# Kernel tuning notes

Measured on AMD Instinct MI355X. Metric: run time of the kernel, lower is better.

Reference implementation:

```python
import jax, jax.numpy as jnp
import numpy as np

EPS = 1e-7


def setup_inputs() -> dict:
    key = jax.random.key(0)
    kx, kw, kv, kp = jax.random.split(key, 4)
    B, H, Wd, d, V, O = 4, 64, 64, 64, 64, 64
    X = jax.random.normal(kx, (B, H, Wd, d), dtype=jnp.float32)
    W = jax.random.normal(kw, (d, V), dtype=jnp.float32)
    # positive variances (kmeans-style init in original); avoid near-zero divisors
    variance = jax.random.uniform(kv, (d, V), dtype=jnp.float32) + 0.5
    weight = jax.random.normal(kp, (d, O), dtype=jnp.float32) * (1.0 / np.sqrt(d))
    return {"X": X, "W": W, "variance": variance, "weight": weight}


def reference(X, W, variance, weight):
    B, H, Wd, d = X.shape
    V = W.shape[1]
    HW = H * Wd
    Xf = X.reshape(B, HW, d)
    # Faithful replication of torch code: extend = tile(X, V) over last axis,
    # then reshape (d*V) -> (d, V) with k = a*V + c, so the X component at
    # grid position (a, c) is X[..., (a*V + c) % d].
    idx = (jnp.arange(d)[:, None] * V + jnp.arange(V)[None, :]) % d  # (d, V)
    Xg = Xf[:, :, idx]                      # (B, HW, d, V)
    q1 = (Xg - W) / variance                # (B, HW, d, V), broadcast (d,V)
    q = jnp.sum(q1 * q1, axis=2)            # (B, HW, V) squared Mahalanobis-ish dist
    q = q - jnp.min(q, axis=-1, keepdims=True)
    Q = jnp.exp(-0.5 * q)
    Q = Q / jnp.sum(Q, axis=-1, keepdims=True)          # soft assignment (B, HW, V)
    # Raw row-major reinterpretation (B, HW, d*V) -> (B, d, HW, V), as in torch
    z = q1.reshape(B, d, HW, V)
    zQ = z * Q[:, None, :, :]                            # (B, d, HW, V)
    z = jnp.sum(zQ, axis=2)                              # (B, d, V)
    Qsum = jnp.sum(Q, axis=1)                            # (B, V)
    z = (z + EPS) / (Qsum[:, None, :] + EPS)
    norm = jnp.sum(z * z, axis=1, keepdims=True)         # (B, 1, V)
    Z = z / norm                                          # (B, d, V)
    Adj = jnp.einsum('bdv,bdu->bvu', Z, Z)               # (B, V, V)
    out = jnp.einsum('bdv,do->bvo', Z, weight)           # (B, V, O)
    out = jnp.einsum('bvu,buo->bvo', Adj, out)           # (B, V, O)
    Zo = jax.nn.relu(out)
    Xn = jnp.einsum('bnv,bvo->bno', Q, Zo)               # (B, HW, O)
    return Xn.reshape(B, H, Wd, -1).transpose(0, 3, 1, 2)  # (B, O, H, W)
```

## Files before the change

### kernel.cpp

```cpp
#include <hip/hip_runtime.h>

#define HW 4096
#define EPSF 1e-7f

#define WS_S1  0
#define WS_S2P 16384
#define WS_QSP 32768
#define WS_Z   49152
#define WS_ZO  65536
#define WS_ABC 81920

__device__ __forceinline__ void xr4(float4& v) {
    v.x += __shfl_xor(v.x, 16); v.y += __shfl_xor(v.y, 16);
    v.z += __shfl_xor(v.z, 16); v.w += __shfl_xor(v.w, 16);
    v.x += __shfl_xor(v.x, 32); v.y += __shfl_xor(v.y, 32);
    v.z += __shfl_xor(v.z, 32); v.w += __shfl_xor(v.w, 32);
}

__device__ __forceinline__ float4 row_softmax(float4 x, float4 A4, float4 B4, float4 C4) {
    float4 q;
    q.x = fmaf(fmaf(A4.x, x.x, -2.0f * B4.x), x.x, C4.x);
    q.y = fmaf(fmaf(A4.y, x.y, -2.0f * B4.y), x.y, C4.y);
    q.z = fmaf(fmaf(A4.z, x.z, -2.0f * B4.z), x.z, C4.z);
    q.w = fmaf(fmaf(A4.w, x.w, -2.0f * B4.w), x.w, C4.w);
    float m = fminf(fminf(q.x, q.y), fminf(q.z, q.w));
    m = fminf(m, __shfl_xor(m, 1)); m = fminf(m, __shfl_xor(m, 2));
    m = fminf(m, __shfl_xor(m, 4)); m = fminf(m, __shfl_xor(m, 8));
    float4 e;
    e.x = __expf(-0.5f * (q.x - m)); e.y = __expf(-0.5f * (q.y - m));
    e.z = __expf(-0.5f * (q.z - m)); e.w = __expf(-0.5f * (q.w - m));
    float s = e.x + e.y + e.z + e.w;
    s += __shfl_xor(s, 1); s += __shfl_xor(s, 2);
    s += __shfl_xor(s, 4); s += __shfl_xor(s, 8);
    float rs = 1.0f / s;
    float4 Q4; Q4.x = e.x * rs; Q4.y = e.y * rs; Q4.z = e.z * rs; Q4.w = e.w * rs;
    return Q4;
}

__global__ __launch_bounds__(512) void kA(const float* __restrict__ X,
                                          const float* __restrict__ Wm,
                                          const float* __restrict__ var,
                                          float* __restrict__ ws) {
    int b = blockIdx.x >> 6, l = blockIdx.x & 63;
    int t = threadIdx.x;
    int wv = t >> 6, j = t & 63;
    int lane16 = t & 15, r0 = t >> 4;
    __shared__ float4 red4[3][8][16];
    __shared__ float4 abc4[3][16];

    float4 iv0, iv1, wiv0, wiv1;
    float4 aA = {0,0,0,0}, aB = {0,0,0,0}, aC = {0,0,0,0};
    {
        float4 v4 = *(const float4*)&var[r0 * 64 + lane16 * 4];
        float4 w4 = *(const float4*)&Wm[r0 * 64 + lane16 * 4];
        iv0.x = 1.0f / v4.x; iv0.y = 1.0f / v4.y; iv0.z = 1.0f / v4.z; iv0.w = 1.0f / v4.w;
        wiv0.x = w4.x * iv0.x; wiv0.y = w4.y * iv0.y; wiv0.z = w4.z * iv0.z; wiv0.w = w4.w * iv0.w;
        aA.x = fmaf(iv0.x, iv0.x, aA.x); aA.y = fmaf(iv0.y, iv0.y, aA.y);
        aA.z = fmaf(iv0.z, iv0.z, aA.z); aA.w = fmaf(iv0.w, iv0.w, aA.w);
        aB.x = fmaf(wiv0.x, iv0.x, aB.x); aB.y = fmaf(wiv0.y, iv0.y, aB.y);
        aB.z = fmaf(wiv0.z, iv0.z, aB.z); aB.w = fmaf(wiv0.w, iv0.w, aB.w);
        aC.x = fmaf(wiv0.x, wiv0.x, aC.x); aC.y = fmaf(wiv0.y, wiv0.y, aC.y);
        aC.z = fmaf(wiv0.z, wiv0.z, aC.z); aC.w = fmaf(wiv0.w, wiv0.w, aC.w);
    }
    {
        int i = r0 + 32;
        float4 v4 = *(const float4*)&var[i * 64 + lane16 * 4];
        float4 w4 = *(const float4*)&Wm[i * 64 + lane16 * 4];
        iv1.x = 1.0f / v4.x; iv1.y = 1.0f / v4.y; iv1.z = 1.0f / v4.z; iv1.w = 1.0f / v4.w;
        wiv1.x = w4.x * iv1.x; wiv1.y = w4.y * iv1.y; wiv1.z = w4.z * iv1.z; wiv1.w = w4.w * iv1.w;
        aA.x = fmaf(iv1.x, iv1.x, aA.x); aA.y = fmaf(iv1.y, iv1.y, aA.y);
        aA.z = fmaf(iv1.z, iv1.z, aA.z); aA.w = fmaf(iv1.w, iv1.w, aA.w);
        aB.x = fmaf(wiv1.x, iv1.x, aB.x); aB.y = fmaf(wiv1.y, iv1.y, aB.y);
        aB.z = fmaf(wiv1.z, iv1.z, aB.z); aB.w = fmaf(wiv1.w, iv1.w, aB.w);
        aC.x = fmaf(wiv1.x, wiv1.x, aC.x); aC.y = fmaf(wiv1.y, wiv1.y, aC.y);
        aC.z = fmaf(wiv1.z, wiv1.z, aC.z); aC.w = fmaf(wiv1.w, wiv1.w, aC.w);
    }
    xr4(aA); xr4(aB); xr4(aC);
    if ((t & 63) < 16) { red4[0][wv][lane16] = aA; red4[1][wv][lane16] = aB; red4[2][wv][lane16] = aC; }
    __syncthreads();
    if (t < 16) {
        float4 A = {0,0,0,0}, Bq = {0,0,0,0}, C = {0,0,0,0};
#pragma unroll
        for (int w = 0; w < 8; w++) {
            float4 a = red4[0][w][t], bb = red4[1][w][t], c = red4[2][w][t];
            A.x += a.x; A.y += a.y; A.z += a.z; A.w += a.w;
            Bq.x += bb.x; Bq.y += bb.y; Bq.z += bb.z; Bq.w += bb.w;
            C.x += c.x; C.y += c.y; C.z += c.z; C.w += c.w;
        }
        abc4[0][t] = A; abc4[1][t] = Bq; abc4[2][t] = C;
        if (blockIdx.x == 0) {
            *(float4*)&ws[WS_ABC + t * 4]       = A;
            *(float4*)&ws[WS_ABC + 64 + t * 4]  = Bq;
            *(float4*)&ws[WS_ABC + 128 + t * 4] = C;
        }
    }
    __syncthreads();
    float4 A4 = abc4[0][lane16], B4 = abc4[1][lane16], C4 = abc4[2][lane16];

    float4 s1 = {0,0,0,0}, s2 = {0,0,0,0}, qsm = {0,0,0,0};
    {
        int n = l * 64 + r0;
        float4 x = *(const float4*)&X[((size_t)(b * HW) + n) * 64 + lane16 * 4];
        float4 Q4 = row_softmax(x, A4, B4, C4);
        s1.x = fmaf(iv0.x, Q4.x, s1.x); s1.y = fmaf(iv0.y, Q4.y, s1.y);
        s1.z = fmaf(iv0.z, Q4.z, s1.z); s1.w = fmaf(iv0.w, Q4.w, s1.w);
        s2.x = fmaf(wiv0.x, Q4.x, s2.x); s2.y = fmaf(wiv0.y, Q4.y, s2.y);
        s2.z = fmaf(wiv0.z, Q4.z, s2.z); s2.w = fmaf(wiv0.w, Q4.w, s2.w);
        qsm.x += Q4.x; qsm.y += Q4.y; qsm.z += Q4.z; qsm.w += Q4.w;
    }
    {
        int n = l * 64 + r0 + 32;
        float4 x = *(const float4*)&X[((size_t)(b * HW) + n) * 64 + lane16 * 4];
        float4 Q4 = row_softmax(x, A4, B4, C4);
        s1.x = fmaf(iv1.x, Q4.x, s1.x); s1.y = fmaf(iv1.y, Q4.y, s1.y);
        s1.z = fmaf(iv1.z, Q4.z, s1.z); s1.w = fmaf(iv1.w, Q4.w, s1.w);
        s2.x = fmaf(wiv1.x, Q4.x, s2.x); s2.y = fmaf(wiv1.y, Q4.y, s2.y);
        s2.z = fmaf(wiv1.z, Q4.z, s2.z); s2.w = fmaf(wiv1.w, Q4.w, s2.w);
        qsm.x += Q4.x; qsm.y += Q4.y; qsm.z += Q4.z; qsm.w += Q4.w;
    }
    xr4(s1); xr4(s2); xr4(qsm);
    __syncthreads();
    if ((t & 63) < 16) { red4[0][wv][lane16] = s1; red4[1][wv][lane16] = s2; red4[2][wv][lane16] = qsm; }
    __syncthreads();
    if (t < 64) {
        int jg = j >> 2, cc = j & 3;
        float t0 = 0.f, t1 = 0.f, t2 = 0.f;
#pragma unroll
        for (int w = 0; w < 8; w++) {
            t0 += ((const float*)&red4[0][w][jg])[cc];
            t1 += ((const float*)&red4[1][w][jg])[cc];
            t2 += ((const float*)&red4[2][w][jg])[cc];
        }
        int idx = (b * 64 + l) * 64 + j;
        ws[WS_S1  + idx] = t0;
        ws[WS_S2P + idx] = t1;
        ws[WS_QSP + idx] = t2;
    }
}

__global__ __launch_bounds__(512) void kB(const float* __restrict__ X,
                                          float* __restrict__ ws) {
    int b = blockIdx.x >> 6, h = blockIdx.x & 63;
    int t = threadIdx.x;
    int wv = t >> 6, j = t & 63;
    int lane16 = t & 15, lg = t >> 4;
    __shared__ float4 red4[3][8][16];
    float4 acc = {0,0,0,0}, ps2 = {0,0,0,0}, pqs = {0,0,0,0};
#pragma unroll
    for (int half = 0; half < 2; half++) {
        int l = lg + half * 32;
        float4 x  = *(const float4*)&X[((size_t)(b * HW) + h * 64 + l) * 64 + lane16 * 4];
        int idx = (b * 64 + l) * 64 + lane16 * 4;
        float4 s1 = *(const float4*)&ws[WS_S1 + idx];
        float4 a2 = *(const float4*)&ws[WS_S2P + idx];
        float4 a3 = *(const float4*)&ws[WS_QSP + idx];
        acc.x = fmaf(x.x, s1.x, acc.x); acc.y = fmaf(x.y, s1.y, acc.y);
        acc.z = fmaf(x.z, s1.z, acc.z); acc.w = fmaf(x.w, s1.w, acc.w);
        ps2.x += a2.x; ps2.y += a2.y; ps2.z += a2.z; ps2.w += a2.w;
        pqs.x += a3.x; pqs.y += a3.y; pqs.z += a3.z; pqs.w += a3.w;
    }
    xr4(acc); xr4(ps2); xr4(pqs);
    if ((t & 63) < 16) {
        red4[0][wv][lane16] = acc; red4[1][wv][lane16] = ps2; red4[2][wv][lane16] = pqs;
    }
    __syncthreads();
    if (t < 64) {
        int jg = j >> 2, cc = j & 3;
        float a = 0.f, s2 = 0.f, q = 0.f;
#pragma unroll
        for (int w = 0; w < 8; w++) {
            a  += ((const float*)&red4[0][w][jg])[cc];
            s2 += ((const float*)&red4[1][w][jg])[cc];
            q  += ((const float*)&red4[2][w][jg])[cc];
        }
        ws[WS_Z + (b * 64 + h) * 64 + j] = (a - s2 + EPSF) / (q + EPSF);
    }
}

__global__ __launch_bounds__(512) void kCD(const float* __restrict__ weight,
                                           float* __restrict__ ws) {
    int b = blockIdx.x >> 6, v = blockIdx.x & 63;
    int w8 = threadIdx.x >> 6, j = threadIdx.x & 63;
    __shared__ float zl[64][65];
    __shared__ float wl[64][65];
    __shared__ float red[8][64];
    __shared__ float sN[64], sin2[64], ghat[64], yv[64];
#pragma unroll
    for (int k = 0; k < 2; k++) {
        int fidx = (k * 512 + threadIdx.x) * 4;
        int r = fidx >> 6, cc = fidx & 63;
        float4 zv = *(const float4*)&ws[WS_Z + b * 4096 + fidx];
        float4 wv = *(const float4*)&weight[fidx];
        zl[r][cc] = zv.x; zl[r][cc+1] = zv.y; zl[r][cc+2] = zv.z; zl[r][cc+3] = zv.w;
        wl[r][cc] = wv.x; wl[r][cc+1] = wv.y; wl[r][cc+2] = wv.z; wl[r][cc+3] = wv.w;
    }
    __syncthreads();
    {
        float na = 0.f;
#pragma unroll
        for (int k = 0; k < 8; k++) { float zz = zl[w8 * 8 + k][j]; na = fmaf(zz, zz, na); }
        red[w8][j] = na;
        __syncthreads();
        if (threadIdx.x < 64) {
            float s = 0.f;
#pragma unroll
            for (int tt = 0; tt < 8; tt++) s += red[tt][j];
            sN[j] = s; sin2[j] = 1.0f / (s * s);
        }
        __syncthreads();
    }
    {
        float g = 0.f;
#pragma unroll
        for (int k = 0; k < 8; k++) { int d = w8 * 8 + k; g = fmaf(zl[d][v], zl[d][j], g); }
        red[w8][j] = g;
        __syncthreads();
        if (threadIdx.x < 64) {
            float s = 0.f;
#pragma unroll
            for (int tt = 0; tt < 8; tt++) s += red[tt][j];
            ghat[j] = s * sin2[j];
        }
        __syncthreads();
    }
    {
        float y = 0.f;
#pragma unroll
        for (int k = 0; k < 8; k++) { int u = w8 * 8 + k; y = fmaf(ghat[u], zl[j][u], y); }
        red[w8][j] = y;
        __syncthreads();
        if (threadIdx.x < 64) {
            float s = 0.f;
#pragma unroll
            for (int tt = 0; tt < 8; tt++) s += red[tt][j];
            yv[j] = s;
        }
        __syncthreads();
    }
    {
        float a = 0.f;
#pragma unroll
        for (int k = 0; k < 8; k++) { int d = w8 * 8 + k; a = fmaf(yv[d], wl[d][j], a); }
        red[w8][j] = a;
        __syncthreads();
        if (threadIdx.x < 64) {
            float s = 0.f;
#pragma unroll
            for (int tt = 0; tt < 8; tt++) s += red[tt][j];
            float r = s / sN[v];
            r = r > 0.f ? r : 0.f;
            ws[WS_ZO + (b * 64 + v) * 64 + j] = r;
        }
    }
}

__global__ __launch_bounds__(512) void kF(const float* __restrict__ X,
                                          const float* __restrict__ ws,
                                          float* __restrict__ out) {
    int b = blockIdx.x >> 6, tb = blockIdx.x & 63;
    int nbase = tb * 64;
    int t = threadIdx.x;
    int w8 = t >> 6, j = t & 63;
    int lane16 = t & 15, r0 = t >> 4;
    int o8 = w8 * 8;
    __shared__ float qs[64][65];
    __shared__ __align__(16) float zo[64][68];

    float4 A4 = *(const float4*)&ws[WS_ABC + lane16 * 4];
    float4 B4 = *(const float4*)&ws[WS_ABC + 64 + lane16 * 4];
    float4 C4 = *(const float4*)&ws[WS_ABC + 128 + lane16 * 4];

#pragma unroll
    for (int k = 0; k < 2; k++) {
        int fidx = (k * 512 + t) * 4;
        int r = fidx >> 6, cc = fidx & 63;
        float4 zv = *(const float4*)&ws[WS_ZO + b * 4096 + fidx];
        zo[r][cc] = zv.x; zo[r][cc+1] = zv.y; zo[r][cc+2] = zv.z; zo[r][cc+3] = zv.w;
    }
#pragma unroll
    for (int half = 0; half < 2; half++) {
        int rr = r0 + half * 32;
        int n = nbase + rr;
        float4 x = *(const float4*)&X[((size_t)(b * HW) + n) * 64 + lane16 * 4];
        float4 Q4 = row_softmax(x, A4, B4, C4);
        qs[rr][lane16 * 4]     = Q4.x;
        qs[rr][lane16 * 4 + 1] = Q4.y;
        qs[rr][lane16 * 4 + 2] = Q4.z;
        qs[rr][lane16 * 4 + 3] = Q4.w;
    }
    __syncthreads();

    float acc[8];
#pragma unroll
    for (int k = 0; k < 8; k++) acc[k] = 0.f;
#pragma unroll
    for (int v = 0; v < 64; v++) {
        float qv = qs[j][v];
        float4 z0 = *(const float4*)&zo[v][o8];
        float4 z1 = *(const float4*)&zo[v][o8 + 4];
        acc[0] = fmaf(qv, z0.x, acc[0]);
        acc[1] = fmaf(qv, z0.y, acc[1]);
        acc[2] = fmaf(qv, z0.z, acc[2]);
        acc[3] = fmaf(qv, z0.w, acc[3]);
        acc[4] = fmaf(qv, z1.x, acc[4]);
        acc[5] = fmaf(qv, z1.y, acc[5]);
        acc[6] = fmaf(qv, z1.z, acc[6]);
        acc[7] = fmaf(qv, z1.w, acc[7]);
    }
#pragma unroll
    for (int k = 0; k < 8; k++) {
        int o = o8 + k;
        out[(size_t)(b * 64 + o) * HW + nbase + j] = acc[k];
    }
}

extern "C" void kernel_launch(void* const* d_in, const int* in_sizes, int n_in,
                              void* d_out, int out_size, void* d_ws, size_t ws_size,
                              hipStream_t stream) {
    const float* X      = (const float*)d_in[0];
    const float* Wm     = (const float*)d_in[1];
    const float* var    = (const float*)d_in[2];
    const float* weight = (const float*)d_in[3];
    float* ws  = (float*)d_ws;
    float* out = (float*)d_out;

    kA <<<256, 512, 0, stream>>>(X, Wm, var, ws);
    kB <<<256, 512, 0, stream>>>(X, ws);
    kCD<<<256, 512, 0, stream>>>(weight, ws);
    kF <<<256, 512, 0, stream>>>(X, ws, out);
}
```

Before: 21.69 us.

## Fuse kB and kCD into one launch with per-batch atomic counters

Merges the Z-reduction kernel and the adjacency/projection kernel into a single 512-block launch. The first 256 blocks compute Z and bump a per-batch counter, and the other 256 blocks spin on that counter before doing the CD work. Counters are zeroed in kA. This removes one kernel launch boundary, but it relies on producer blocks being scheduled before or alongside the spinning consumer blocks, and polling adds its own latency.

```diff
diff --git a/kernel.cpp b/kernel.cpp
--- a/kernel.cpp
+++ b/kernel.cpp
@@ -9,6 +9,7 @@
 #define WS_Z   49152
 #define WS_ZO  65536
 #define WS_ABC 81920
+#define WS_CTR 82176
 
 __device__ __forceinline__ void xr4(float4& v) {
     v.x += __shfl_xor(v.x, 16); v.y += __shfl_xor(v.y, 16);
@@ -48,6 +49,8 @@
     __shared__ float4 red4[3][8][16];
     __shared__ float4 abc4[3][16];
 
+    if (blockIdx.x == 0 && t < 8) ((int*)(ws + WS_CTR))[t] = 0;
+
     float4 iv0, iv1, wiv0, wiv1;
     float4 aA = {0,0,0,0}, aB = {0,0,0,0}, aC = {0,0,0,0};
     {
@@ -138,116 +141,137 @@
     }
 }
 
-__global__ __launch_bounds__(512) void kB(const float* __restrict__ X,
-                                          float* __restrict__ ws) {
-    int b = blockIdx.x >> 6, h = blockIdx.x & 63;
-    int t = threadIdx.x;
-    int wv = t >> 6, j = t & 63;
-    int lane16 = t & 15, lg = t >> 4;
-    __shared__ float4 red4[3][8][16];
-    float4 acc = {0,0,0,0}, ps2 = {0,0,0,0}, pqs = {0,0,0,0};
-#pragma unroll
-    for (int half = 0; half < 2; half++) {
-        int l = lg + half * 32;
-        float4 x  = *(const float4*)&X[((size_t)(b * HW) + h * 64 + l) * 64 + lane16 * 4];
-        int idx = (b * 64 + l) * 64 + lane16 * 4;
-        float4 s1 = *(const float4*)&ws[WS_S1 + idx];
-        float4 a2 = *(const float4*)&ws[WS_S2P + idx];
-        float4 a3 = *(const float4*)&ws[WS_QSP + idx];
-        acc.x = fmaf(x.x, s1.x, acc.x); acc.y = fmaf(x.y, s1.y, acc.y);
-        acc.z = fmaf(x.z, s1.z, acc.z); acc.w = fmaf(x.w, s1.w, acc.w);
-        ps2.x += a2.x; ps2.y += a2.y; ps2.z += a2.z; ps2.w += a2.w;
-        pqs.x += a3.x; pqs.y += a3.y; pqs.z += a3.z; pqs.w += a3.w;
-    }
-    xr4(acc); xr4(ps2); xr4(pqs);
-    if ((t & 63) < 16) {
-        red4[0][wv][lane16] = acc; red4[1][wv][lane16] = ps2; red4[2][wv][lane16] = pqs;
-    }
-    __syncthreads();
-    if (t < 64) {
-        int jg = j >> 2, cc = j & 3;
-        float a = 0.f, s2 = 0.f, q = 0.f;
-#pragma unroll
-        for (int w = 0; w < 8; w++) {
-            a  += ((const float*)&red4[0][w][jg])[cc];
-            s2 += ((const float*)&red4[1][w][jg])[cc];
-            q  += ((const float*)&red4[2][w][jg])[cc];
-        }
-        ws[WS_Z + (b * 64 + h) * 64 + j] = (a - s2 + EPSF) / (q + EPSF);
-    }
-}
-
-__global__ __launch_bounds__(512) void kCD(const float* __restrict__ weight,
-                                           float* __restrict__ ws) {
-    int b = blockIdx.x >> 6, v = blockIdx.x & 63;
-    int w8 = threadIdx.x >> 6, j = threadIdx.x & 63;
-    __shared__ float zl[64][65];
-    __shared__ float wl[64][65];
-    __shared__ float red[8][64];
-    __shared__ float sN[64], sin2[64], ghat[64], yv[64];
+struct BRole { float4 red4[3][8][16]; };
+struct CDRole {
+    float zl[64][65]; float wl[64][65];
+    float red[8][64];
+    float sN[64]; float sin2[64]; float ghat[64]; float yv[64];
+};
+union SMU { BRole b; CDRole c; };
+
+__global__ __launch_bounds__(512) void kBCD(const float* __restrict__ X,
+                                            const float* __restrict__ weight,
+                                            float* __restrict__ ws) {
+    __shared__ SMU sm;
+    int* ctr = (int*)(ws + WS_CTR);
+    const int t = threadIdx.x;
+
+    if (blockIdx.x < 256) {
+        int b = blockIdx.x >> 6, h = blockIdx.x & 63;
+        int wv = t >> 6, j = t & 63;
+        int lane16 = t & 15, lg = t >> 4;
+        float4 acc = {0,0,0,0}, ps2 = {0,0,0,0}, pqs = {0,0,0,0};
+#pragma unroll
+        for (int half = 0; half < 2; half++) {
+            int l = lg + half * 32;
+            float4 x  = *(const float4*)&X[((size_t)(b * HW) + h * 64 + l) * 64 + lane16 * 4];
+            int idx = (b * 64 + l) * 64 + lane16 * 4;
+            float4 s1 = *(const float4*)&ws[WS_S1 + idx];
+            float4 a2 = *(const float4*)&ws[WS_S2P + idx];
+            float4 a3 = *(const float4*)&ws[WS_QSP + idx];
+            acc.x = fmaf(x.x, s1.x, acc.x); acc.y = fmaf(x.y, s1.y, acc.y);
+            acc.z = fmaf(x.z, s1.z, acc.z); acc.w = fmaf(x.w, s1.w, acc.w);
+            ps2.x += a2.x; ps2.y += a2.y; ps2.z += a2.z; ps2.w += a2.w;
+            pqs.x += a3.x; pqs.y += a3.y; pqs.z += a3.z; pqs.w += a3.w;
+        }
+        xr4(acc); xr4(ps2); xr4(pqs);
+        if ((t & 63) < 16) {
+            sm.b.red4[0][wv][lane16] = acc; sm.b.red4[1][wv][lane16] = ps2; sm.b.red4[2][wv][lane16] = pqs;
+        }
+        __syncthreads();
+        if (t < 64) {
+            int jg = j >> 2, cc = j & 3;
+            float a = 0.f, s2 = 0.f, q = 0.f;
+#pragma unroll
+            for (int w = 0; w < 8; w++) {
+                a  += ((const float*)&sm.b.red4[0][w][jg])[cc];
+                s2 += ((const float*)&sm.b.red4[1][w][jg])[cc];
+                q  += ((const float*)&sm.b.red4[2][w][jg])[cc];
+            }
+            ws[WS_Z + (b * 64 + h) * 64 + j] = (a - s2 + EPSF) / (q + EPSF);
+        }
+        __syncthreads();
+        if (t == 0) {
+            __threadfence();
+            __hip_atomic_fetch_add(ctr + b, 1, __ATOMIC_RELAXED, __HIP_MEMORY_SCOPE_AGENT);
+        }
+        return;
+    }
+
+    int m = blockIdx.x - 256;
+    int b = m >> 6, v = m & 63;
+    int w8 = t >> 6, j = t & 63;
+    if (t == 0) {
+        while (__hip_atomic_load(ctr + b, __ATOMIC_RELAXED, __HIP_MEMORY_SCOPE_AGENT) < 64) {
+            __builtin_amdgcn_s_sleep(32);
+        }
+        __threadfence();
+    }
+    __syncthreads();
+
 #pragma unroll
     for (int k = 0; k < 2; k++) {
-        int fidx = (k * 512 + threadIdx.x) * 4;
+        int fidx = (k * 512 + t) * 4;
         int r = fidx >> 6, cc = fidx & 63;
         float4 zv = *(const float4*)&ws[WS_Z + b * 4096 + fidx];
         float4 wv = *(const float4*)&weight[fidx];
-        zl[r][cc] = zv.x; zl[r][cc+1] = zv.y; zl[r][cc+2] = zv.z; zl[r][cc+3] = zv.w;
-        wl[r][cc] = wv.x; wl[r][cc+1] = wv.y; wl[r][cc+2] = wv.z; wl[r][cc+3] = wv.w;
+        sm.c.zl[r][cc] = zv.x; sm.c.zl[r][cc+1] = zv.y; sm.c.zl[r][cc+2] = zv.z; sm.c.zl[r][cc+3] = zv.w;
+        sm.c.wl[r][cc] = wv.x; sm.c.wl[r][cc+1] = wv.y; sm.c.wl[r][cc+2] = wv.z; sm.c.wl[r][cc+3] = wv.w;
     }
     __syncthreads();
     {
         float na = 0.f;
 #pragma unroll
-        for (int k = 0; k < 8; k++) { float zz = zl[w8 * 8 + k][j]; na = fmaf(zz, zz, na); }
-        red[w8][j] = na;
-        __syncthreads();
-        if (threadIdx.x < 64) {
+        for (int k = 0; k < 8; k++) { float zz = sm.c.zl[w8 * 8 + k][j]; na = fmaf(zz, zz, na); }
+        sm.c.red[w8][j] = na;
+        __syncthreads();
+        if (t < 64) {
             float s = 0.f;
 #pragma unroll
-            for (int tt = 0; tt < 8; tt++) s += red[tt][j];
-            sN[j] = s; sin2[j] = 1.0f / (s * s);
+            for (int tt = 0; tt < 8; tt++) s += sm.c.red[tt][j];
+            sm.c.sN[j] = s; sm.c.sin2[j] = 1.0f / (s * s);
         }
         __syncthreads();
     }
     {
         float g = 0.f;
 #pragma unroll
-        for (int k = 0; k < 8; k++) { int d = w8 * 8 + k; g = fmaf(zl[d][v], zl[d][j], g); }
-        red[w8][j] = g;
-        __syncthreads();
-        if (threadIdx.x < 64) {
+        for (int k = 0; k < 8; k++) { int d = w8 * 8 + k; g = fmaf(sm.c.zl[d][v], sm.c.zl[d][j], g); }
+        sm.c.red[w8][j] = g;
+        __syncthreads();
+        if (t < 64) {
             float s = 0.f;
 #pragma unroll
-            for (int tt = 0; tt < 8; tt++) s += red[tt][j];
-            ghat[j] = s * sin2[j];
+            for (int tt = 0; tt < 8; tt++) s += sm.c.red[tt][j];
+            sm.c.ghat[j] = s * sm.c.sin2[j];
         }
         __syncthreads();
     }
     {
         float y = 0.f;
 #pragma unroll
-        for (int k = 0; k < 8; k++) { int u = w8 * 8 + k; y = fmaf(ghat[u], zl[j][u], y); }
-        red[w8][j] = y;
-        __syncthreads();
-        if (threadIdx.x < 64) {
+        for (int k = 0; k < 8; k++) { int u = w8 * 8 + k; y = fmaf(sm.c.ghat[u], sm.c.zl[j][u], y); }
+        sm.c.red[w8][j] = y;
+        __syncthreads();
+        if (t < 64) {
             float s = 0.f;
 #pragma unroll
-            for (int tt = 0; tt < 8; tt++) s += red[tt][j];
-            yv[j] = s;
+            for (int tt = 0; tt < 8; tt++) s += sm.c.red[tt][j];
+            sm.c.yv[j] = s;
         }
         __syncthreads();
     }
     {
         float a = 0.f;
 #pragma unroll
-        for (int k = 0; k < 8; k++) { int d = w8 * 8 + k; a = fmaf(yv[d], wl[d][j], a); }
-        red[w8][j] = a;
-        __syncthreads();
-        if (threadIdx.x < 64) {
+        for (int k = 0; k < 8; k++) { int d = w8 * 8 + k; a = fmaf(sm.c.yv[d], sm.c.wl[d][j], a); }
+        sm.c.red[w8][j] = a;
+        __syncthreads();
+        if (t < 64) {
             float s = 0.f;
 #pragma unroll
-            for (int tt = 0; tt < 8; tt++) s += red[tt][j];
-            float r = s / sN[v];
+            for (int tt = 0; tt < 8; tt++) s += sm.c.red[tt][j];
+            float r = s / sm.c.sN[v];
             r = r > 0.f ? r : 0.f;
             ws[WS_ZO + (b * 64 + v) * 64 + j] = r;
         }
@@ -324,8 +348,7 @@
     float* ws  = (float*)d_ws;
     float* out = (float*)d_out;
 
-    kA <<<256, 512, 0, stream>>>(X, Wm, var, ws);
-    kB <<<256, 512, 0, stream>>>(X, ws);
-    kCD<<<256, 512, 0, stream>>>(weight, ws);
-    kF <<<256, 512, 0, stream>>>(X, ws, out);
-}
+    kA  <<<256, 512, 0, stream>>>(X, Wm, var, ws);
+    kBCD<<<512, 512, 0, stream>>>(X, weight, ws);
+    kF  <<<256, 512, 0, stream>>>(X, ws, out);
+}
```

After: 35.05 us. +61.6%, slower.
